# Kernel tuning notes

Measured on AMD Instinct MI355X. Metric: run time of the kernel, lower is better.

## Reference

```python
import jax, jax.numpy as jnp
import numpy as np

NUM_BINS = 15
NUM_CLASSES = 4
NEIGHBORHOOD_WIDTH = 3  # K; num_neighbor_classes = K**2 = 9


def _neighbor_counts(onehot):
    """Count of same-class neighbors in KxK window (center excluded), zero padding.
    onehot: [B, C, H, W] float32 one-hot of hard predictions.
    returns int32 [B, C, H, W] in [0, K^2-1].
    """
    K = NEIGHBORHOOD_WIDTH
    C = onehot.shape[1]
    kern = np.ones((K, K), dtype=np.float32)
    kern[K // 2, K // 2] = 0.0  # exclude center pixel
    kernel = jnp.asarray(np.broadcast_to(kern, (C, 1, K, K)).copy())  # depthwise OIHW
    counts = jax.lax.conv_general_dilated(
        onehot, kernel,
        window_strides=(1, 1), padding='SAME',
        feature_group_count=C,
        dimension_numbers=('NCHW', 'OIHW', 'NCHW'))
    return jnp.clip(jnp.round(counts).astype(jnp.int32), 0, K * K - 1)


def setup_inputs() -> dict:
    key = jax.random.key(0)
    k1, k2 = jax.random.split(key)
    logits = jax.random.normal(k1, (16, NUM_CLASSES, 512, 512), dtype=jnp.float32)
    # calibration frequency table: val_freqs[class][neighbor_count][conf_bin]
    val_freqs = jax.random.uniform(k2, (NUM_CLASSES, NEIGHBORHOOD_WIDTH ** 2, NUM_BINS), dtype=jnp.float32)
    return {"logits": logits, "val_freqs": val_freqs}


def reference(logits, val_freqs):
    B, C, H, W = logits.shape
    probs = jax.nn.softmax(logits, axis=1)                      # [B,C,H,W]
    y_hard = jnp.argmax(probs, axis=1)                          # [B,H,W]

    # (y_hard == lab_idx) for every class at once -> one-hot [B,C,H,W]
    onehot = jax.nn.one_hot(y_hard, C, axis=1, dtype=jnp.float32)
    agg = _neighbor_counts(onehot)                              # [B,C,H,W] int32 in [0, K^2-1]

    # confidence bin per pixel/class: uniform bins on [0,1]
    bin_width = 1.0 / NUM_BINS
    bin_map = jnp.clip((probs / bin_width).astype(jnp.int32), 0, NUM_BINS - 1)  # [B,C,H,W]

    # fused multi-index gather replacing the nested class/neighbor-mask loops:
    # calibrated[b,c,h,w] = val_freqs[c, agg[b,c,h,w], bin_map[b,c,h,w]]
    cls_idx = jnp.arange(C, dtype=jnp.int32)[None, :, None, None]
    calibrated = val_freqs[cls_idx, agg, bin_map]               # [B,C,H,W]

    # normalize across classes, guarding zero sums
    s = jnp.sum(calibrated, axis=1, keepdims=True)
    s = jnp.where(s == 0, 1.0, s)
    return calibrated / s
```

## Files before the change

### kernel.cpp

```cpp
#include <hip/hip_runtime.h>

#define HW (512 * 512)

typedef float vfloat4 __attribute__((ext_vector_type(4)));
typedef float vfloat2 __attribute__((ext_vector_type(2)));
typedef unsigned int vuint4 __attribute__((ext_vector_type(4)));

constexpr int CWP = 516;
constexpr float BWIDTH = 1.0f / 15.0f;
constexpr float DELTA = 3e-5f;

__global__ __launch_bounds__(512) void nectar_binning_kernel(
    const float* __restrict__ logits,
    const float* __restrict__ val_freqs,
    float* __restrict__ out)
{
    __shared__ unsigned int cls[6 * CWP];
    __shared__ float vf[540];

    const unsigned int f = blockIdx.x;
    const unsigned int l = ((f & 7u) << 8) | (f >> 3);
    const int panel = (int)(l & 127u);
    const int b     = (int)(l >> 7);
    const int h0  = panel * 4;
    const int tid = (int)threadIdx.x;

    for (int i = tid; i < 540; i += 512) vf[i] = val_freqs[i];
    if (tid < 6) { cls[tid * CWP] = 0u; cls[tid * CWP + 513] = 0u; }

    const float* lb = logits + (size_t)b * 4 * HW;

    const int r = tid >> 7;
    const int t = tid & 127;
    const int w = 4 * t;
    const int base = ((h0 + r) << 9) + w;

    vfloat4 xa[4];
    #pragma unroll
    for (int c = 0; c < 4; c++)
        xa[c] = *reinterpret_cast<const vfloat4*>(lb + (size_t)c * HW + base);

    const int hrow = tid >> 8;
    const int p = tid & 255;
    const int hh = hrow ? (h0 + 4) : (h0 - 1);
    const bool hv = (unsigned)hh < 512u;
    vfloat2 hx[4];
    #pragma unroll
    for (int c = 0; c < 4; c++) { hx[c].x = 0.f; hx[c].y = 0.f; }
    if (hv) {
        const int hb = (hh << 9) + 2 * p;
        #pragma unroll
        for (int c = 0; c < 4; c++)
            hx[c] = *reinterpret_cast<const vfloat2*>(lb + (size_t)c * HW + hb);
    }

    auto px_phase1 = [&](float x0, float x1, float x2, float x3,
                         int clsaddr) -> unsigned int {
        int c = 0; float best = x0;
        if (x1 > best) { best = x1; c = 1; }
        if (x2 > best) { best = x2; c = 2; }
        if (x3 > best) { best = x3; c = 3; }
        cls[clsaddr] = 1u << (4 * c);

        float m = fmaxf(fmaxf(x0, x1), fmaxf(x2, x3));
        float t0 = x0 - m, t1 = x1 - m, t2 = x2 - m, t3 = x3 - m;
        float f0 = __expf(t0), f1 = __expf(t1), f2 = __expf(t2), f3 = __expf(t3);
        float sf = ((f0 + f1) + f2) + f3;
        float rs = __builtin_amdgcn_rcpf(sf);
        float q[4];
        q[0] = (f0 * rs) * 15.0f; q[1] = (f1 * rs) * 15.0f;
        q[2] = (f2 * rs) * 15.0f; q[3] = (f3 * rs) * 15.0f;
        bool slow = false;
        #pragma unroll
        for (int c2 = 0; c2 < 4; c2++) {
            float fr = q[c2] - floorf(q[c2]);
            slow |= (fr < DELTA) | (fr > 1.0f - DELTA);
        }
        if (slow) {
            float e0 = expf(t0), e1 = expf(t1), e2 = expf(t2), e3 = expf(t3);
            float s = ((e0 + e1) + e2) + e3;
            q[0] = (e0 / s) / BWIDTH; q[1] = (e1 / s) / BWIDTH;
            q[2] = (e2 / s) / BWIDTH; q[3] = (e3 / s) / BWIDTH;
        }
        unsigned int pb = 0;
        #pragma unroll
        for (int c2 = 0; c2 < 4; c2++) {
            int bin = (int)q[c2];
            bin = bin > 14 ? 14 : bin;
            pb |= (unsigned int)bin << (4 * c2);
        }
        return pb;
    };

    unsigned int pbin[4];
    #pragma unroll
    for (int j = 0; j < 4; j++)
        pbin[j] = px_phase1(xa[0][j], xa[1][j], xa[2][j], xa[3][j],
                            (r + 1) * CWP + 1 + w + j);

    {
        unsigned int v0 = 0, v1 = 0;
        if (hv) {
            int c = 0; float best = hx[0].x;
            if (hx[1].x > best) { best = hx[1].x; c = 1; }
            if (hx[2].x > best) { best = hx[2].x; c = 2; }
            if (hx[3].x > best) { best = hx[3].x; c = 3; }
            v0 = 1u << (4 * c);
            c = 0; best = hx[0].y;
            if (hx[1].y > best) { best = hx[1].y; c = 1; }
            if (hx[2].y > best) { best = hx[2].y; c = 2; }
            if (hx[3].y > best) { best = hx[3].y; c = 3; }
            v1 = 1u << (4 * c);
        }
        const int hl = hrow * 5 * CWP + 1 + 2 * p;
        cls[hl]     = v0;
        cls[hl + 1] = v1;
    }
    __syncthreads();

    const unsigned int* p0 = &cls[r * CWP + w];
    vuint4 ra[3], rb[3];
    #pragma unroll
    for (int k = 0; k < 3; k++) {
        ra[k] = *reinterpret_cast<const vuint4*>(p0 + k * CWP);
        rb[k] = *reinterpret_cast<const vuint4*>(p0 + k * CWP + 4);
    }
    unsigned int colsum[6], mid[6];
    #pragma unroll
    for (int k = 0; k < 6; k++) {
        unsigned int a0 = (k < 4) ? ra[0][k] : rb[0][k - 4];
        unsigned int a1 = (k < 4) ? ra[1][k] : rb[1][k - 4];
        unsigned int a2 = (k < 4) ? ra[2][k] : rb[2][k - 4];
        mid[k] = a1;
        colsum[k] = a0 + a1 + a2;
    }

    float res[4][4];
    #pragma unroll
    for (int j = 0; j < 4; j++) {
        unsigned int pk = colsum[j] + colsum[j + 1] + colsum[j + 2] - mid[j + 1];
        unsigned int pb = pbin[j];
        float cs = 0.0f;
        float cal[4];
        #pragma unroll
        for (int c = 0; c < 4; c++) {
            int cnt = (int)((pk >> (4 * c)) & 0xFu);
            int bin = (int)((pb >> (4 * c)) & 0xFu);
            float v = vf[c * 135 + cnt * 15 + bin];
            cal[c] = v;
            cs += v;
        }
        if (cs == 0.0f) cs = 1.0f;
        float inv = __builtin_amdgcn_rcpf(cs);
        #pragma unroll
        for (int c = 0; c < 4; c++) res[c][j] = cal[c] * inv;
    }

    float* ob = out + (size_t)b * 4 * HW + base;
    #pragma unroll
    for (int c = 0; c < 4; c++) {
        vfloat4 v;
        v.x = res[c][0]; v.y = res[c][1]; v.z = res[c][2]; v.w = res[c][3];
        __builtin_nontemporal_store(v, reinterpret_cast<vfloat4*>(ob + (size_t)c * HW));
    }
}

extern "C" void kernel_launch(void* const* d_in, const int* in_sizes, int n_in,
                              void* d_out, int out_size, void* d_ws, size_t ws_size,
                              hipStream_t stream) {
    const float* logits    = (const float*)d_in[0];
    const float* val_freqs = (const float*)d_in[1];
    float* out             = (float*)d_out;

    dim3 block(512, 1, 1);
    dim3 grid(2048, 1, 1);
    hipLaunchKernelGGL(nectar_binning_kernel, grid, block, 0, stream,
                       logits, val_freqs, out);
}
```

Baseline: 110.9 us.

## Halve block size and process two 2-row sub-panels per thread

Blocks drop from 512 to 256 threads. Each thread now computes two output rows, in two 2-row sub-panels that have separate shared-memory class buffers, and issues all logit loads for both sub-panels up front. The aim is more work and memory-level parallelism per thread, with the second sub-panel's loads overlapping the first sub-panel's phase-1 math. In exchange, each block now reads four halo rows instead of two, and two of those are interior rows loaded again. It also adds an extra barrier and raises register pressure.

```diff
diff --git a/kernel.cpp b/kernel.cpp
--- a/kernel.cpp
+++ b/kernel.cpp
@@ -3,64 +3,70 @@
 #define HW (512 * 512)
 
 typedef float vfloat4 __attribute__((ext_vector_type(4)));
-typedef float vfloat2 __attribute__((ext_vector_type(2)));
 typedef unsigned int vuint4 __attribute__((ext_vector_type(4)));
 
 constexpr int CWP = 516;
 constexpr float BWIDTH = 1.0f / 15.0f;
 constexpr float DELTA = 3e-5f;
 
-__global__ __launch_bounds__(512) void nectar_binning_kernel(
+__global__ __launch_bounds__(256) void nectar_binning_kernel(
     const float* __restrict__ logits,
     const float* __restrict__ val_freqs,
     float* __restrict__ out)
 {
-    __shared__ unsigned int cls[6 * CWP];
+    __shared__ unsigned int cls0[4 * CWP];
+    __shared__ unsigned int cls1[4 * CWP];
     __shared__ float vf[540];
 
     const unsigned int f = blockIdx.x;
     const unsigned int l = ((f & 7u) << 8) | (f >> 3);
-    const int panel = (int)(l & 127u);
-    const int b     = (int)(l >> 7);
-    const int h0  = panel * 4;
+    const int pp = (int)(l & 127u);
+    const int b  = (int)(l >> 7);
+    const int h0  = pp * 4;
     const int tid = (int)threadIdx.x;
 
-    for (int i = tid; i < 540; i += 512) vf[i] = val_freqs[i];
-    if (tid < 6) { cls[tid * CWP] = 0u; cls[tid * CWP + 513] = 0u; }
+    for (int i = tid; i < 540; i += 256) vf[i] = val_freqs[i];
+    if (tid < 4)      { cls0[tid * CWP] = 0u; cls0[tid * CWP + 513] = 0u; }
+    else if (tid < 8) { cls1[(tid - 4) * CWP] = 0u; cls1[(tid - 4) * CWP + 513] = 0u; }
 
     const float* lb = logits + (size_t)b * 4 * HW;
 
     const int r = tid >> 7;
     const int t = tid & 127;
     const int w = 4 * t;
-    const int base = ((h0 + r) << 9) + w;
+    const int base0 = ((h0 + r) << 9) + w;
+    const int base1 = base0 + 1024;
 
-    vfloat4 xa[4];
+    vfloat4 xa[4], hx[4], xb[4];
     #pragma unroll
     for (int c = 0; c < 4; c++)
-        xa[c] = *reinterpret_cast<const vfloat4*>(lb + (size_t)c * HW + base);
+        xa[c] = *reinterpret_cast<const vfloat4*>(lb + (size_t)c * HW + base0);
 
-    const int hrow = tid >> 8;
-    const int p = tid & 255;
-    const int hh = hrow ? (h0 + 4) : (h0 - 1);
-    const bool hv = (unsigned)hh < 512u;
-    vfloat2 hx[4];
+    const int hh0 = r ? (h0 + 2) : (h0 - 1);
+    const bool hv0 = (unsigned)hh0 < 512u;
     #pragma unroll
-    for (int c = 0; c < 4; c++) { hx[c].x = 0.f; hx[c].y = 0.f; }
-    if (hv) {
-        const int hb = (hh << 9) + 2 * p;
+    for (int c = 0; c < 4; c++) { vfloat4 z = {0.f, 0.f, 0.f, 0.f}; hx[c] = z; }
+    if (hv0) {
+        const int hb = (hh0 << 9) + w;
         #pragma unroll
         for (int c = 0; c < 4; c++)
-            hx[c] = *reinterpret_cast<const vfloat2*>(lb + (size_t)c * HW + hb);
+            hx[c] = *reinterpret_cast<const vfloat4*>(lb + (size_t)c * HW + hb);
     }
+    #pragma unroll
+    for (int c = 0; c < 4; c++)
+        xb[c] = *reinterpret_cast<const vfloat4*>(lb + (size_t)c * HW + base1);
 
-    auto px_phase1 = [&](float x0, float x1, float x2, float x3,
-                         int clsaddr) -> unsigned int {
+    auto argnib = [](float x0, float x1, float x2, float x3) -> unsigned int {
         int c = 0; float best = x0;
         if (x1 > best) { best = x1; c = 1; }
         if (x2 > best) { best = x2; c = 2; }
         if (x3 > best) { best = x3; c = 3; }
-        cls[clsaddr] = 1u << (4 * c);
+        return 1u << (4 * c);
+    };
+
+    auto px_phase1 = [&](float x0, float x1, float x2, float x3,
+                         unsigned int* clsbuf, int clsaddr) -> unsigned int {
+        clsbuf[clsaddr] = argnib(x0, x1, x2, x3);
 
         float m = fmaxf(fmaxf(x0, x1), fmaxf(x2, x3));
         float t0 = x0 - m, t1 = x1 - m, t2 = x2 - m, t3 = x3 - m;
@@ -92,77 +98,87 @@
         return pb;
     };
 
-    unsigned int pbin[4];
+    auto phase2 = [&](const unsigned int* clsbuf, const unsigned int* pbin, float* ob) {
+        const unsigned int* p0 = &clsbuf[r * CWP + w];
+        vuint4 ra[3], rb[3];
+        #pragma unroll
+        for (int k = 0; k < 3; k++) {
+            ra[k] = *reinterpret_cast<const vuint4*>(p0 + k * CWP);
+            rb[k] = *reinterpret_cast<const vuint4*>(p0 + k * CWP + 4);
+        }
+        unsigned int colsum[6], mid[6];
+        #pragma unroll
+        for (int k = 0; k < 6; k++) {
+            unsigned int a0 = (k < 4) ? ra[0][k] : rb[0][k - 4];
+            unsigned int a1 = (k < 4) ? ra[1][k] : rb[1][k - 4];
+            unsigned int a2 = (k < 4) ? ra[2][k] : rb[2][k - 4];
+            mid[k] = a1;
+            colsum[k] = a0 + a1 + a2;
+        }
+
+        float res[4][4];
+        #pragma unroll
+        for (int j = 0; j < 4; j++) {
+            unsigned int pk = colsum[j] + colsum[j + 1] + colsum[j + 2] - mid[j + 1];
+            unsigned int pb = pbin[j];
+            float cs = 0.0f;
+            float cal[4];
+            #pragma unroll
+            for (int c = 0; c < 4; c++) {
+                int cnt = (int)((pk >> (4 * c)) & 0xFu);
+                int bin = (int)((pb >> (4 * c)) & 0xFu);
+                float v = vf[c * 135 + cnt * 15 + bin];
+                cal[c] = v;
+                cs += v;
+            }
+            if (cs == 0.0f) cs = 1.0f;
+            float inv = __builtin_amdgcn_rcpf(cs);
+            #pragma unroll
+            for (int c = 0; c < 4; c++) res[c][j] = cal[c] * inv;
+        }
+        #pragma unroll
+        for (int c = 0; c < 4; c++) {
+            vfloat4 v;
+            v.x = res[c][0]; v.y = res[c][1]; v.z = res[c][2]; v.w = res[c][3];
+            __builtin_nontemporal_store(v, reinterpret_cast<vfloat4*>(ob + (size_t)c * HW));
+        }
+    };
+
+    const int ia = (r + 1) * CWP + 1 + w;
+    const int ha = (r ? 3 : 0) * CWP + 1 + w;
+    unsigned int pbin0[4];
     #pragma unroll
     for (int j = 0; j < 4; j++)
-        pbin[j] = px_phase1(xa[0][j], xa[1][j], xa[2][j], xa[3][j],
-                            (r + 1) * CWP + 1 + w + j);
+        pbin0[j] = px_phase1(xa[0][j], xa[1][j], xa[2][j], xa[3][j], cls0, ia + j);
+    #pragma unroll
+    for (int j = 0; j < 4; j++)
+        cls0[ha + j] = hv0 ? argnib(hx[0][j], hx[1][j], hx[2][j], hx[3][j]) : 0u;
 
-    {
-        unsigned int v0 = 0, v1 = 0;
-        if (hv) {
-            int c = 0; float best = hx[0].x;
-            if (hx[1].x > best) { best = hx[1].x; c = 1; }
-            if (hx[2].x > best) { best = hx[2].x; c = 2; }
-            if (hx[3].x > best) { best = hx[3].x; c = 3; }
-            v0 = 1u << (4 * c);
-            c = 0; best = hx[0].y;
-            if (hx[1].y > best) { best = hx[1].y; c = 1; }
-            if (hx[2].y > best) { best = hx[2].y; c = 2; }
-            if (hx[3].y > best) { best = hx[3].y; c = 3; }
-            v1 = 1u << (4 * c);
-        }
-        const int hl = hrow * 5 * CWP + 1 + 2 * p;
-        cls[hl]     = v0;
-        cls[hl + 1] = v1;
+    const int hh1 = r ? (h0 + 4) : (h0 + 1);
+    const bool hv1 = (unsigned)hh1 < 512u;
+    vfloat4 hy[4];
+    #pragma unroll
+    for (int c = 0; c < 4; c++) { vfloat4 z = {0.f, 0.f, 0.f, 0.f}; hy[c] = z; }
+    if (hv1) {
+        const int hb = (hh1 << 9) + w;
+        #pragma unroll
+        for (int c = 0; c < 4; c++)
+            hy[c] = *reinterpret_cast<const vfloat4*>(lb + (size_t)c * HW + hb);
     }
     __syncthreads();
 
-    const unsigned int* p0 = &cls[r * CWP + w];
-    vuint4 ra[3], rb[3];
+    unsigned int pbin1[4];
     #pragma unroll
-    for (int k = 0; k < 3; k++) {
-        ra[k] = *reinterpret_cast<const vuint4*>(p0 + k * CWP);
-        rb[k] = *reinterpret_cast<const vuint4*>(p0 + k * CWP + 4);
-    }
-    unsigned int colsum[6], mid[6];
+    for (int j = 0; j < 4; j++)
+        pbin1[j] = px_phase1(xb[0][j], xb[1][j], xb[2][j], xb[3][j], cls1, ia + j);
     #pragma unroll
-    for (int k = 0; k < 6; k++) {
-        unsigned int a0 = (k < 4) ? ra[0][k] : rb[0][k - 4];
-        unsigned int a1 = (k < 4) ? ra[1][k] : rb[1][k - 4];
-        unsigned int a2 = (k < 4) ? ra[2][k] : rb[2][k - 4];
-        mid[k] = a1;
-        colsum[k] = a0 + a1 + a2;
-    }
+    for (int j = 0; j < 4; j++)
+        cls1[ha + j] = hv1 ? argnib(hy[0][j], hy[1][j], hy[2][j], hy[3][j]) : 0u;
 
-    float res[4][4];
-    #pragma unroll
-    for (int j = 0; j < 4; j++) {
-        unsigned int pk = colsum[j] + colsum[j + 1] + colsum[j + 2] - mid[j + 1];
-        unsigned int pb = pbin[j];
-        float cs = 0.0f;
-        float cal[4];
-        #pragma unroll
-        for (int c = 0; c < 4; c++) {
-            int cnt = (int)((pk >> (4 * c)) & 0xFu);
-            int bin = (int)((pb >> (4 * c)) & 0xFu);
-            float v = vf[c * 135 + cnt * 15 + bin];
-            cal[c] = v;
-            cs += v;
-        }
-        if (cs == 0.0f) cs = 1.0f;
-        float inv = __builtin_amdgcn_rcpf(cs);
-        #pragma unroll
-        for (int c = 0; c < 4; c++) res[c][j] = cal[c] * inv;
-    }
-
-    float* ob = out + (size_t)b * 4 * HW + base;
-    #pragma unroll
-    for (int c = 0; c < 4; c++) {
-        vfloat4 v;
-        v.x = res[c][0]; v.y = res[c][1]; v.z = res[c][2]; v.w = res[c][3];
-        __builtin_nontemporal_store(v, reinterpret_cast<vfloat4*>(ob + (size_t)c * HW));
-    }
+    float* obase = out + (size_t)b * 4 * HW;
+    phase2(cls0, pbin0, obase + base0);
+    __syncthreads();
+    phase2(cls1, pbin1, obase + base1);
 }
 
 extern "C" void kernel_launch(void* const* d_in, const int* in_sizes, int n_in,
@@ -172,7 +188,7 @@
     const float* val_freqs = (const float*)d_in[1];
     float* out             = (float*)d_out;
 
-    dim3 block(512, 1, 1);
+    dim3 block(256, 1, 1);
     dim3 grid(2048, 1, 1);
     hipLaunchKernelGGL(nectar_binning_kernel, grid, block, 0, stream,
                        logits, val_freqs, out);
```

Measured after the change: 114.4 us. 3.1% more time.

## Split into pack kernel and gather kernel via packed workspace

Applied to the files above, without the earlier changes.

Replaces the single fused kernel with two kernels when a workspace is available. The first computes argmax and confidence bins per pixel and packs them into one 32-bit word. The second reads three packed rows per wave, builds neighbor counts with nibble arithmetic and wave shuffles, then does the table lookup and normalization. This avoids the shared-memory halo staging and the halo logit loads, at the cost of an extra 16 MB workspace write and read plus a second launch. The fused kernel stays as a fallback.

```diff
diff --git a/kernel.cpp b/kernel.cpp
--- a/kernel.cpp
+++ b/kernel.cpp
@@ -3,14 +3,185 @@
 #define HW (512 * 512)
 
 typedef float vfloat4 __attribute__((ext_vector_type(4)));
-typedef float vfloat2 __attribute__((ext_vector_type(2)));
 typedef unsigned int vuint4 __attribute__((ext_vector_type(4)));
 
-constexpr int CWP = 516;
 constexpr float BWIDTH = 1.0f / 15.0f;
 constexpr float DELTA = 3e-5f;
 
-__global__ __launch_bounds__(512) void nectar_binning_kernel(
+
+__global__ __launch_bounds__(256) void nectar_k1_pack(
+    const float* __restrict__ logits,
+    unsigned* __restrict__ cmp)
+{
+    const int gid = (int)(blockIdx.x * 256 + threadIdx.x);
+    const int b   = gid >> 16;
+    const int off = (gid & 65535) << 2;
+
+    const float* lb = logits + (size_t)b * 4 * HW + off;
+    vfloat4 x0 = *reinterpret_cast<const vfloat4*>(lb);
+    vfloat4 x1 = *reinterpret_cast<const vfloat4*>(lb + HW);
+    vfloat4 x2 = *reinterpret_cast<const vfloat4*>(lb + 2 * HW);
+    vfloat4 x3 = *reinterpret_cast<const vfloat4*>(lb + 3 * HW);
+
+    vuint4 o;
+    #pragma unroll
+    for (int j = 0; j < 4; j++) {
+        float a0 = x0[j], a1 = x1[j], a2 = x2[j], a3 = x3[j];
+        int c = 0; float best = a0;
+        if (a1 > best) { best = a1; c = 1; }
+        if (a2 > best) { best = a2; c = 2; }
+        if (a3 > best) { best = a3; c = 3; }
+
+        float m = fmaxf(fmaxf(a0, a1), fmaxf(a2, a3));
+        float t0 = a0 - m, t1 = a1 - m, t2 = a2 - m, t3 = a3 - m;
+        float f0 = __expf(t0), f1 = __expf(t1), f2 = __expf(t2), f3 = __expf(t3);
+        float sf = ((f0 + f1) + f2) + f3;
+        float rs = __builtin_amdgcn_rcpf(sf);
+        float q[4];
+        q[0] = (f0 * rs) * 15.0f; q[1] = (f1 * rs) * 15.0f;
+        q[2] = (f2 * rs) * 15.0f; q[3] = (f3 * rs) * 15.0f;
+        bool slow = false;
+        #pragma unroll
+        for (int c2 = 0; c2 < 4; c2++) {
+            float fr = q[c2] - floorf(q[c2]);
+            slow |= (fr < DELTA) | (fr > 1.0f - DELTA);
+        }
+        if (slow) {
+            float e0 = expf(t0), e1 = expf(t1), e2 = expf(t2), e3 = expf(t3);
+            float s = ((e0 + e1) + e2) + e3;
+            q[0] = (e0 / s) / BWIDTH; q[1] = (e1 / s) / BWIDTH;
+            q[2] = (e2 / s) / BWIDTH; q[3] = (e3 / s) / BWIDTH;
+        }
+        unsigned pb = 0;
+        #pragma unroll
+        for (int c2 = 0; c2 < 4; c2++) {
+            int bin = (int)q[c2];
+            bin = bin > 14 ? 14 : bin;
+            pb |= (unsigned)bin << (4 * c2);
+        }
+        o[j] = pb | ((unsigned)c << 16);
+    }
+    *reinterpret_cast<vuint4*>(cmp + (size_t)b * HW + off) = o;
+}
+
+__global__ __launch_bounds__(256) void nectar_k2_gather(
+    const unsigned* __restrict__ cmp,
+    const float* __restrict__ val_freqs,
+    float* __restrict__ out)
+{
+    __shared__ float vf[540];
+
+    const int tid  = (int)threadIdx.x;
+    const int lane = tid & 63;
+    const int wv   = tid >> 6;
+
+    float vfr[9];
+    #pragma unroll
+    for (int i = 0; i < 9; i++) {
+        int idx = 64 * i + lane;
+        vfr[i] = (idx < 540) ? val_freqs[idx] : 0.f;
+    }
+
+    const unsigned bi  = blockIdx.x;
+    const unsigned bsw = ((bi & 7u) << 8) | (bi >> 3);
+    const int seg = (int)(4u * bsw) + wv;
+    const int b   = seg >> 9;
+    const int row = seg & 511;
+
+    const unsigned* cb = cmp + (size_t)b * HW;
+    float*          ob = out + (size_t)b * 4 * HW;
+    const int colA = 4 * lane;
+    const int colB = 256 + 4 * lane;
+
+    vuint4 tA, tB, mA, mB, bA, bB;
+    {
+        const unsigned* rp = cb + ((row > 0 ? row - 1 : 0) << 9);
+        tA = *reinterpret_cast<const vuint4*>(rp + colA);
+        tB = *reinterpret_cast<const vuint4*>(rp + colB);
+        rp = cb + (row << 9);
+        mA = *reinterpret_cast<const vuint4*>(rp + colA);
+        mB = *reinterpret_cast<const vuint4*>(rp + colB);
+        rp = cb + ((row < 511 ? row + 1 : 511) << 9);
+        bA = *reinterpret_cast<const vuint4*>(rp + colA);
+        bB = *reinterpret_cast<const vuint4*>(rp + colB);
+    }
+    #pragma unroll
+    for (int i = 0; i < 9; i++) {
+        int idx = 64 * i + lane;
+        if (idx < 540) vf[idx] = vfr[i];
+    }
+
+    auto NIBW = [](unsigned w0, unsigned w1) -> unsigned {
+        return (1u << (4 * ((w0 >> 16) & 3u))) | ((1u << (4 * ((w1 >> 16) & 3u))) << 16);
+    };
+    unsigned T[2][2] = {{NIBW(tA.x, tA.y), NIBW(tA.z, tA.w)},
+                        {NIBW(tB.x, tB.y), NIBW(tB.z, tB.w)}};
+    unsigned M[2][2] = {{NIBW(mA.x, mA.y), NIBW(mA.z, mA.w)},
+                        {NIBW(mB.x, mB.y), NIBW(mB.z, mB.w)}};
+    unsigned B[2][2] = {{NIBW(bA.x, bA.y), NIBW(bA.z, bA.w)},
+                        {NIBW(bB.x, bB.y), NIBW(bB.z, bB.w)}};
+    if (row == 0)   { T[0][0] = T[0][1] = T[1][0] = T[1][1] = 0; }
+    if (row == 511) { B[0][0] = B[0][1] = B[1][0] = B[1][1] = 0; }
+    const unsigned P[2][2] = {
+        {(mA.x & 0xFFFFu) | ((mA.y & 0xFFFFu) << 16), (mA.z & 0xFFFFu) | ((mA.w & 0xFFFFu) << 16)},
+        {(mB.x & 0xFFFFu) | ((mB.y & 0xFFFFu) << 16), (mB.z & 0xFFFFu) | ((mB.w & 0xFFFFu) << 16)}};
+
+    unsigned C[2][2];
+    #pragma unroll
+    for (int h = 0; h < 2; h++) {
+        C[h][0] = T[h][0] + M[h][0] + B[h][0];
+        C[h][1] = T[h][1] + M[h][1] + B[h][1];
+    }
+    unsigned upA = __shfl_up(C[0][1], 1) >> 16;   if (lane == 0)  upA = 0;
+    unsigned ebA = __shfl(C[0][1], 63) >> 16;
+    unsigned upB = __shfl_up(C[1][1], 1) >> 16;   if (lane == 0)  upB = ebA;
+    unsigned e0B = __shfl(C[1][0], 0) & 0xFFFFu;
+    unsigned dnA = __shfl_down(C[0][0], 1) & 0xFFFFu; if (lane == 63) dnA = e0B;
+    unsigned dnB = __shfl_down(C[1][0], 1) & 0xFFFFu; if (lane == 63) dnB = 0;
+    const unsigned up[2] = {upA, upB}, dn[2] = {dnA, dnB};
+
+    float res[4][2][4];
+    #pragma unroll
+    for (int h = 0; h < 2; h++) {
+        unsigned L0 = (C[h][0] << 16) | up[h];
+        unsigned R0 = (C[h][0] >> 16) | (C[h][1] << 16);
+        unsigned R1 = (C[h][1] >> 16) | (dn[h] << 16);
+        unsigned PKw[2];
+        PKw[0] = C[h][0] + L0 + R0 - M[h][0];
+        PKw[1] = C[h][1] + R0 + R1 - M[h][1];
+        #pragma unroll
+        for (int j = 0; j < 4; j++) {
+            unsigned pk = (PKw[j >> 1]  >> (16 * (j & 1))) & 0xFFFFu;
+            unsigned pb = (P[h][j >> 1] >> (16 * (j & 1))) & 0xFFFFu;
+            float cs = 0.0f;
+            float cal[4];
+            #pragma unroll
+            for (int c = 0; c < 4; c++) {
+                int cnt = (int)((pk >> (4 * c)) & 0xFu);
+                int bin = (int)((pb >> (4 * c)) & 0xFu);
+                float v = vf[c * 135 + cnt * 15 + bin];
+                cal[c] = v;
+                cs += v;
+            }
+            if (cs == 0.0f) cs = 1.0f;
+            float inv = __builtin_amdgcn_rcpf(cs);
+            #pragma unroll
+            for (int c = 0; c < 4; c++) res[c][h][j] = cal[c] * inv;
+        }
+    }
+    float* rp = ob + (row << 9);
+    #pragma unroll
+    for (int c = 0; c < 4; c++) {
+        vfloat4 v0; v0.x = res[c][0][0]; v0.y = res[c][0][1]; v0.z = res[c][0][2]; v0.w = res[c][0][3];
+        vfloat4 v1; v1.x = res[c][1][0]; v1.y = res[c][1][1]; v1.z = res[c][1][2]; v1.w = res[c][1][3];
+        __builtin_nontemporal_store(v0, reinterpret_cast<vfloat4*>(rp + (size_t)c * HW + colA));
+        __builtin_nontemporal_store(v1, reinterpret_cast<vfloat4*>(rp + (size_t)c * HW + colB));
+    }
+}
+
+constexpr int CWP = 516;
+
+__global__ __launch_bounds__(512) void nectar_binning_fused(
     const float* __restrict__ logits,
     const float* __restrict__ val_freqs,
     float* __restrict__ out)
@@ -44,14 +215,16 @@
     const int p = tid & 255;
     const int hh = hrow ? (h0 + 4) : (h0 - 1);
     const bool hv = (unsigned)hh < 512u;
-    vfloat2 hx[4];
-    #pragma unroll
-    for (int c = 0; c < 4; c++) { hx[c].x = 0.f; hx[c].y = 0.f; }
+    float hx[4][2];
+    #pragma unroll
+    for (int c = 0; c < 4; c++) { hx[c][0] = 0.f; hx[c][1] = 0.f; }
     if (hv) {
         const int hb = (hh << 9) + 2 * p;
         #pragma unroll
-        for (int c = 0; c < 4; c++)
-            hx[c] = *reinterpret_cast<const vfloat2*>(lb + (size_t)c * HW + hb);
+        for (int c = 0; c < 4; c++) {
+            hx[c][0] = lb[(size_t)c * HW + hb];
+            hx[c][1] = lb[(size_t)c * HW + hb + 1];
+        }
     }
 
     auto px_phase1 = [&](float x0, float x1, float x2, float x3,
@@ -101,15 +274,15 @@
     {
         unsigned int v0 = 0, v1 = 0;
         if (hv) {
-            int c = 0; float best = hx[0].x;
-            if (hx[1].x > best) { best = hx[1].x; c = 1; }
-            if (hx[2].x > best) { best = hx[2].x; c = 2; }
-            if (hx[3].x > best) { best = hx[3].x; c = 3; }
+            int c = 0; float best = hx[0][0];
+            if (hx[1][0] > best) { best = hx[1][0]; c = 1; }
+            if (hx[2][0] > best) { best = hx[2][0]; c = 2; }
+            if (hx[3][0] > best) { best = hx[3][0]; c = 3; }
             v0 = 1u << (4 * c);
-            c = 0; best = hx[0].y;
-            if (hx[1].y > best) { best = hx[1].y; c = 1; }
-            if (hx[2].y > best) { best = hx[2].y; c = 2; }
-            if (hx[3].y > best) { best = hx[3].y; c = 3; }
+            c = 0; best = hx[0][1];
+            if (hx[1][1] > best) { best = hx[1][1]; c = 1; }
+            if (hx[2][1] > best) { best = hx[2][1]; c = 2; }
+            if (hx[3][1] > best) { best = hx[3][1]; c = 3; }
             v1 = 1u << (4 * c);
         }
         const int hl = hrow * 5 * CWP + 1 + 2 * p;
@@ -172,8 +345,15 @@
     const float* val_freqs = (const float*)d_in[1];
     float* out             = (float*)d_out;
 
-    dim3 block(512, 1, 1);
-    dim3 grid(2048, 1, 1);
-    hipLaunchKernelGGL(nectar_binning_kernel, grid, block, 0, stream,
-                       logits, val_freqs, out);
+    const size_t needed = (size_t)16 * HW * sizeof(unsigned);
+    if (d_ws != nullptr && ws_size >= needed) {
+        unsigned* cmp = (unsigned*)d_ws;
+        hipLaunchKernelGGL(nectar_k1_pack, dim3(4096), dim3(256), 0, stream,
+                           logits, cmp);
+        hipLaunchKernelGGL(nectar_k2_gather, dim3(2048), dim3(256), 0, stream,
+                           cmp, val_freqs, out);
+    } else {
+        hipLaunchKernelGGL(nectar_binning_fused, dim3(2048), dim3(512), 0, stream,
+                           logits, val_freqs, out);
+    }
 }
```

After: 117.4 us. 1.06x slower.

## Process four row-panels per block with double-buffered LDS and prefetched loads

Applied to the files above, without the earlier changes.

Each block now handles a 16-row band as four 4-row panels instead of a single panel. The grid shrinks from 2048 to 512 blocks, and the val_freqs table load and setup are amortized across panels. The next panel's logits are loaded into registers while the current one is processed, and the class-map LDS buffer alternates between two copies so only one barrier is needed per panel. This aims to hide global-load latency and cut per-block overhead, at the cost of higher register use and fewer blocks to spread across the GPU's CUs.

```diff
diff --git a/kernel.cpp b/kernel.cpp
--- a/kernel.cpp
+++ b/kernel.cpp
@@ -15,52 +15,53 @@
     const float* __restrict__ val_freqs,
     float* __restrict__ out)
 {
-    __shared__ unsigned int cls[6 * CWP];
+    __shared__ unsigned int cls[2][6 * CWP];
     __shared__ float vf[540];
 
     const unsigned int f = blockIdx.x;
-    const unsigned int l = ((f & 7u) << 8) | (f >> 3);
-    const int panel = (int)(l & 127u);
-    const int b     = (int)(l >> 7);
-    const int h0  = panel * 4;
-    const int tid = (int)threadIdx.x;
+    const unsigned int l = ((f & 7u) << 6) | (f >> 3);
+    const int b    = (int)(l >> 5);
+    const int band = (int)(l & 31u);
+    const int hb0  = band << 4;
+    const int tid  = (int)threadIdx.x;
 
     for (int i = tid; i < 540; i += 512) vf[i] = val_freqs[i];
-    if (tid < 6) { cls[tid * CWP] = 0u; cls[tid * CWP + 513] = 0u; }
-
-    const float* lb = logits + (size_t)b * 4 * HW;
+    if (tid < 6)       { cls[0][tid * CWP] = 0u; cls[0][tid * CWP + 513] = 0u; }
+    else if (tid < 12) { cls[1][(tid - 6) * CWP] = 0u; cls[1][(tid - 6) * CWP + 513] = 0u; }
+
+    const float* lb    = logits + (size_t)b * 4 * HW;
+    float*       obase = out    + (size_t)b * 4 * HW;
 
     const int r = tid >> 7;
     const int t = tid & 127;
     const int w = 4 * t;
-    const int base = ((h0 + r) << 9) + w;
-
-    vfloat4 xa[4];
-    #pragma unroll
-    for (int c = 0; c < 4; c++)
-        xa[c] = *reinterpret_cast<const vfloat4*>(lb + (size_t)c * HW + base);
-
     const int hrow = tid >> 8;
     const int p = tid & 255;
-    const int hh = hrow ? (h0 + 4) : (h0 - 1);
-    const bool hv = (unsigned)hh < 512u;
-    vfloat2 hx[4];
-    #pragma unroll
-    for (int c = 0; c < 4; c++) { hx[c].x = 0.f; hx[c].y = 0.f; }
-    if (hv) {
-        const int hb = (hh << 9) + 2 * p;
+
+    auto LOADP = [&](int h0, vfloat4 (&xa)[4], vfloat2 (&hx)[4], bool &hv) {
+        const int base = ((h0 + r) << 9) + w;
         #pragma unroll
         for (int c = 0; c < 4; c++)
-            hx[c] = *reinterpret_cast<const vfloat2*>(lb + (size_t)c * HW + hb);
-    }
+            xa[c] = *reinterpret_cast<const vfloat4*>(lb + (size_t)c * HW + base);
+        const int hh = hrow ? (h0 + 4) : (h0 - 1);
+        hv = (unsigned)hh < 512u;
+        #pragma unroll
+        for (int c = 0; c < 4; c++) { hx[c].x = 0.f; hx[c].y = 0.f; }
+        if (hv) {
+            const int hbp = (hh << 9) + 2 * p;
+            #pragma unroll
+            for (int c = 0; c < 4; c++)
+                hx[c] = *reinterpret_cast<const vfloat2*>(lb + (size_t)c * HW + hbp);
+        }
+    };
 
     auto px_phase1 = [&](float x0, float x1, float x2, float x3,
-                         int clsaddr) -> unsigned int {
+                         unsigned int* clsbuf, int clsaddr) -> unsigned int {
         int c = 0; float best = x0;
         if (x1 > best) { best = x1; c = 1; }
         if (x2 > best) { best = x2; c = 2; }
         if (x3 > best) { best = x3; c = 3; }
-        cls[clsaddr] = 1u << (4 * c);
+        clsbuf[clsaddr] = 1u << (4 * c);
 
         float m = fmaxf(fmaxf(x0, x1), fmaxf(x2, x3));
         float t0 = x0 - m, t1 = x1 - m, t2 = x2 - m, t3 = x3 - m;
@@ -92,13 +93,12 @@
         return pb;
     };
 
-    unsigned int pbin[4];
-    #pragma unroll
-    for (int j = 0; j < 4; j++)
-        pbin[j] = px_phase1(xa[0][j], xa[1][j], xa[2][j], xa[3][j],
-                            (r + 1) * CWP + 1 + w + j);
-
-    {
+    auto PH1 = [&](const vfloat4 (&xa)[4], const vfloat2 (&hx)[4], bool hv,
+                   unsigned int* clsbuf, unsigned int (&pbin)[4]) {
+        #pragma unroll
+        for (int j = 0; j < 4; j++)
+            pbin[j] = px_phase1(xa[0][j], xa[1][j], xa[2][j], xa[3][j],
+                                clsbuf, (r + 1) * CWP + 1 + w + j);
         unsigned int v0 = 0, v1 = 0;
         if (hv) {
             int c = 0; float best = hx[0].x;
@@ -113,56 +113,83 @@
             v1 = 1u << (4 * c);
         }
         const int hl = hrow * 5 * CWP + 1 + 2 * p;
-        cls[hl]     = v0;
-        cls[hl + 1] = v1;
-    }
-    __syncthreads();
-
-    const unsigned int* p0 = &cls[r * CWP + w];
-    vuint4 ra[3], rb[3];
-    #pragma unroll
-    for (int k = 0; k < 3; k++) {
-        ra[k] = *reinterpret_cast<const vuint4*>(p0 + k * CWP);
-        rb[k] = *reinterpret_cast<const vuint4*>(p0 + k * CWP + 4);
-    }
-    unsigned int colsum[6], mid[6];
-    #pragma unroll
-    for (int k = 0; k < 6; k++) {
-        unsigned int a0 = (k < 4) ? ra[0][k] : rb[0][k - 4];
-        unsigned int a1 = (k < 4) ? ra[1][k] : rb[1][k - 4];
-        unsigned int a2 = (k < 4) ? ra[2][k] : rb[2][k - 4];
-        mid[k] = a1;
-        colsum[k] = a0 + a1 + a2;
-    }
-
-    float res[4][4];
-    #pragma unroll
-    for (int j = 0; j < 4; j++) {
-        unsigned int pk = colsum[j] + colsum[j + 1] + colsum[j + 2] - mid[j + 1];
-        unsigned int pb = pbin[j];
-        float cs = 0.0f;
-        float cal[4];
+        clsbuf[hl]     = v0;
+        clsbuf[hl + 1] = v1;
+    };
+
+    auto PH2 = [&](int h0, const unsigned int* clsbuf, const unsigned int (&pbin)[4]) {
+        const unsigned int* p0 = &clsbuf[r * CWP + w];
+        vuint4 ra[3], rb[3];
+        #pragma unroll
+        for (int k = 0; k < 3; k++) {
+            ra[k] = *reinterpret_cast<const vuint4*>(p0 + k * CWP);
+            rb[k] = *reinterpret_cast<const vuint4*>(p0 + k * CWP + 4);
+        }
+        unsigned int colsum[6], mid[6];
+        #pragma unroll
+        for (int k = 0; k < 6; k++) {
+            unsigned int a0 = (k < 4) ? ra[0][k] : rb[0][k - 4];
+            unsigned int a1 = (k < 4) ? ra[1][k] : rb[1][k - 4];
+            unsigned int a2 = (k < 4) ? ra[2][k] : rb[2][k - 4];
+            mid[k] = a1;
+            colsum[k] = a0 + a1 + a2;
+        }
+
+        float res[4][4];
+        #pragma unroll
+        for (int j = 0; j < 4; j++) {
+            unsigned int pk = colsum[j] + colsum[j + 1] + colsum[j + 2] - mid[j + 1];
+            unsigned int pb = pbin[j];
+            float cs = 0.0f;
+            float cal[4];
+            #pragma unroll
+            for (int c = 0; c < 4; c++) {
+                int cnt = (int)((pk >> (4 * c)) & 0xFu);
+                int bin = (int)((pb >> (4 * c)) & 0xFu);
+                float v = vf[c * 135 + cnt * 15 + bin];
+                cal[c] = v;
+                cs += v;
+            }
+            if (cs == 0.0f) cs = 1.0f;
+            float inv = __builtin_amdgcn_rcpf(cs);
+            #pragma unroll
+            for (int c = 0; c < 4; c++) res[c][j] = cal[c] * inv;
+        }
+
+        float* ob = obase + (((h0 + r) << 9) + w);
         #pragma unroll
         for (int c = 0; c < 4; c++) {
-            int cnt = (int)((pk >> (4 * c)) & 0xFu);
-            int bin = (int)((pb >> (4 * c)) & 0xFu);
-            float v = vf[c * 135 + cnt * 15 + bin];
-            cal[c] = v;
-            cs += v;
-        }
-        if (cs == 0.0f) cs = 1.0f;
-        float inv = __builtin_amdgcn_rcpf(cs);
-        #pragma unroll
-        for (int c = 0; c < 4; c++) res[c][j] = cal[c] * inv;
-    }
-
-    float* ob = out + (size_t)b * 4 * HW + base;
-    #pragma unroll
-    for (int c = 0; c < 4; c++) {
-        vfloat4 v;
-        v.x = res[c][0]; v.y = res[c][1]; v.z = res[c][2]; v.w = res[c][3];
-        __builtin_nontemporal_store(v, reinterpret_cast<vfloat4*>(ob + (size_t)c * HW));
-    }
+            vfloat4 v;
+            v.x = res[c][0]; v.y = res[c][1]; v.z = res[c][2]; v.w = res[c][3];
+            __builtin_nontemporal_store(v, reinterpret_cast<vfloat4*>(ob + (size_t)c * HW));
+        }
+    };
+
+    vfloat4 xA[4], xB[4];
+    vfloat2 hA[4], hB[4];
+    bool vA, vB;
+    unsigned int pbin[4];
+
+    LOADP(hb0, xA, hA, vA);
+
+    LOADP(hb0 + 4, xB, hB, vB);
+    PH1(xA, hA, vA, cls[0], pbin);
+    __syncthreads();
+    PH2(hb0, cls[0], pbin);
+
+    LOADP(hb0 + 8, xA, hA, vA);
+    PH1(xB, hB, vB, cls[1], pbin);
+    __syncthreads();
+    PH2(hb0 + 4, cls[1], pbin);
+
+    LOADP(hb0 + 12, xB, hB, vB);
+    PH1(xA, hA, vA, cls[0], pbin);
+    __syncthreads();
+    PH2(hb0 + 8, cls[0], pbin);
+
+    PH1(xB, hB, vB, cls[1], pbin);
+    __syncthreads();
+    PH2(hb0 + 12, cls[1], pbin);
 }
 
 extern "C" void kernel_launch(void* const* d_in, const int* in_sizes, int n_in,
@@ -173,7 +200,7 @@
     float* out             = (float*)d_out;
 
     dim3 block(512, 1, 1);
-    dim3 grid(2048, 1, 1);
+    dim3 grid(512, 1, 1);
     hipLaunchKernelGGL(nectar_binning_kernel, grid, block, 0, stream,
                        logits, val_freqs, out);
 }
```

Result: slower. 118.4 us (+6.7%).
